# Kernel optimization log

Measured on AMD Instinct MI355X. Metric: run time of the kernel, lower is better.

The kernel has to match this reference:

```python
import jax, jax.numpy as jnp
import numpy as np


def setup_inputs() -> dict:
    key = jax.random.key(0)
    ks = jax.random.split(key, 8)
    B, T, D, S, M = 32, 512, 1024, 256, 10
    scale = 1.0 / np.sqrt(D)
    return {
        "input_h_c": jax.random.normal(ks[0], (B, T, D), dtype=jnp.float32),
        "memory": jax.random.normal(ks[1], (B, S, D), dtype=jnp.float32),
        "input_lengths": jax.random.randint(ks[2], (B,), 1, S),
        "W_ih": jax.random.normal(ks[3], (4 * D, 2 * D), dtype=jnp.float32) * scale,
        "W_hh": jax.random.normal(ks[4], (4 * D, D), dtype=jnp.float32) * scale,
        "b_ih": jnp.zeros((4 * D,), dtype=jnp.float32),
        "b_hh": jnp.zeros((4 * D,), dtype=jnp.float32),
        "W_g": jax.random.normal(ks[5], (3 * M, D), dtype=jnp.float32) * scale,
        "b_g": jnp.zeros((3 * M,), dtype=jnp.float32),
    }


def reference(input_h_c, memory, input_lengths, W_ih, W_hh, b_ih, b_hh, W_g, b_g):
    B, T, D = input_h_c.shape
    S = memory.shape[1]
    M = W_g.shape[0] // 3
    u = jnp.arange(S, dtype=jnp.float32)
    u_R = u + 0.5  # [S]
    u_L = u - 0.5

    def step(carry, inp_t):
        h, c, ksi, ctx = carry
        x = jnp.concatenate([inp_t, ctx], axis=-1)  # [B, 2D]
        gates = x @ W_ih.T + b_ih + h @ W_hh.T + b_hh  # [B, 4D]
        i_g, f_g, g_g, o_g = jnp.split(gates, 4, axis=-1)
        c = jax.nn.sigmoid(f_g) * c + jax.nn.sigmoid(i_g) * jnp.tanh(g_g)
        h = jax.nn.sigmoid(o_g) * jnp.tanh(c)
        phi = h @ W_g.T + b_g  # [B, 3M]
        ksi = jnp.minimum(ksi + jnp.exp(phi[:, :M]), S - 1.0)
        beta = jnp.exp(phi[:, M:2 * M])
        alpha = jax.nn.softmax(phi[:, 2 * M:], axis=-1)
        # F(u) = 1/(1+exp((ksi-u)/beta)) = sigmoid((u-ksi)/beta)
        ks_e = ksi[:, :, None]   # [B,M,1]
        be_e = beta[:, :, None]
        term1 = jnp.einsum('bm,bms->bs', alpha, jax.nn.sigmoid((u_R - ks_e) / be_e))
        term2 = jnp.einsum('bm,bms->bs', alpha, jax.nn.sigmoid((u_L - ks_e) / be_e))
        w = term1 - term2  # [B,S]
        w = w / jnp.sum(w, axis=-1, keepdims=True)
        ctx = jnp.einsum('bs,bsd->bd', w, memory)  # [B,D]
        terminate = 1.0 - term1  # [B,S]
        return (h, c, ksi, ctx), (ctx, w, terminate)

    init = (jnp.zeros((B, D), input_h_c.dtype), jnp.zeros((B, D), input_h_c.dtype),
            jnp.zeros((B, M), input_h_c.dtype), jnp.zeros((B, D), input_h_c.dtype))
    (h, c, ksi, ctx), (ctxs, ws, terms) = jax.lax.scan(step, init, jnp.swapaxes(input_h_c, 0, 1))
    alignment = jnp.swapaxes(ws, 0, 1)  # [B,T,S]
    term_last = terms[-1]  # [B,S] (last timestep, as in torch loop)
    idx = jnp.clip(input_lengths - 1, 0, memory.shape[1] - 1)
    termination = jnp.take_along_axis(term_last, idx[:, None], axis=1)  # [B,1]
    return (ctx[:, None, :], alignment, termination)
```

## Files before the change

### kernel.cpp

```cpp
#include <hip/hip_runtime.h>
#include <cstdint>
#include <cstddef>

#define B_   32
#define T_   512
#define D_   1024
#define S_   256
#define M_   10
#define G4   4096
#define K3   3072
#define NBLK 256
#define NTHR 256

#define AL_OFF   32768
#define TERM_OFF (32768 + (size_t)B_*T_*S_)

__device__ __forceinline__ void gbar(unsigned* bar, unsigned g) {
    __syncthreads();
    if (threadIdx.x == 0) {
        __threadfence();
        const int grp = blockIdx.x & 7;
        unsigned* cnt  = bar + 32*grp;
        unsigned* cntm = bar + 256;
        unsigned* gen  = bar + 512 + 32*grp;
        bool done = false;
        unsigned old = __hip_atomic_fetch_add(cnt, 1u, __ATOMIC_ACQ_REL, __HIP_MEMORY_SCOPE_AGENT);
        if (old == 31u) {
            unsigned old2 = __hip_atomic_fetch_add(cntm, 1u, __ATOMIC_ACQ_REL, __HIP_MEMORY_SCOPE_AGENT);
            if (old2 == 7u) {
                for (int i = 0; i < 8; ++i)
                    __hip_atomic_store(bar + 32*i, 0u, __ATOMIC_RELAXED, __HIP_MEMORY_SCOPE_AGENT);
                __hip_atomic_store(cntm, 0u, __ATOMIC_RELAXED, __HIP_MEMORY_SCOPE_AGENT);
                for (int i = 0; i < 8; ++i)
                    __hip_atomic_store(bar + 512 + 32*i, g + 1u, __ATOMIC_RELEASE, __HIP_MEMORY_SCOPE_AGENT);
                done = true;
            }
        }
        if (!done) {
            while (__hip_atomic_load(gen, __ATOMIC_RELAXED, __HIP_MEMORY_SCOPE_AGENT) == g)
                __builtin_amdgcn_s_sleep(2);
        }
        __threadfence();
    }
    __syncthreads();
}

__global__ __launch_bounds__(256) void k_pack(const float* __restrict__ Wih,
                                              const float* __restrict__ Whh,
                                              float* __restrict__ WrecT) {
    const int kt = blockIdx.x;
    const int jt = blockIdx.y;
    __shared__ float Tt[32][33];
    const int r = threadIdx.x >> 3;
    const int q = threadIdx.x & 7;
    const int j = jt*32 + r;
    const int k = kt*32 + q*4;
    float4 v;
    if (k < 2048) v = *(const float4*)&Wih[(size_t)j*2048 + k];
    else          v = *(const float4*)&Whh[(size_t)j*1024 + (k - 2048)];
    Tt[r][q*4+0] = v.x; Tt[r][q*4+1] = v.y; Tt[r][q*4+2] = v.z; Tt[r][q*4+3] = v.w;
    __syncthreads();
    float4 o;
    o.x = Tt[q*4+0][r]; o.y = Tt[q*4+1][r]; o.z = Tt[q*4+2][r]; o.w = Tt[q*4+3][r];
    *(float4*)&WrecT[(size_t)(kt*32 + r)*G4 + jt*32 + q*4] = o;
}

__global__ __launch_bounds__(256) void k_bsum(const float* __restrict__ bih,
                                              const float* __restrict__ bhh,
                                              float* __restrict__ bsum,
                                              unsigned* __restrict__ bar) {
    int i = blockIdx.x*256 + threadIdx.x;
    if (i < G4) bsum[i] = bih[i] + bhh[i];
    if (blockIdx.x == 0)
        for (int j = threadIdx.x; j < 1024; j += 256) bar[j] = 0u;
}

__global__ __launch_bounds__(NTHR, 1) void k_rec(
    const float* __restrict__ inp,
    const float* __restrict__ mem,
    const int*   __restrict__ lens,
    const float* __restrict__ Wg,
    const float* __restrict__ bg,
    const float* __restrict__ WrecT,
    const float* __restrict__ bsum,
    float* __restrict__ xh,
    float* __restrict__ cst,
    float* __restrict__ ksi,
    float* __restrict__ part,
    float* __restrict__ wcur,
    unsigned* __restrict__ bar,
    float* __restrict__ out)
{
    __shared__ __align__(16) float smem[5632];
    const int blk = blockIdx.x;
    const int tid = threadIdx.x;
    unsigned bgen = 0;

    if (blk < B_) {
        for (int i = tid; i < 2*D_; i += NTHR) xh[blk*2*D_ + i] = 0.f;
        for (int i = tid; i < D_; i += NTHR)   cst[blk*D_ + i]  = 0.f;
        if (tid < M_) ksi[blk*16 + tid] = 0.f;
    }
    gbar(bar, bgen); ++bgen;

    for (int t = 0; t < T_; ++t) {
        {
            const int kc = blk & 7;
            const int jb = blk >> 3;
            const int jbase = jb * 128;
            const int tx = tid & 31;
            const int ty = tid >> 5;
            const int sb = tid >> 3;
            const int sk = tid & 7;
            float* Ws = smem;
            float* Xs = smem + 32*132;
            float acc[4][4] = {{0.f}};
            float4 xv, wv[4];

            auto loadX = [&](int kbase) {
                if (kbase < D_) xv = *(const float4*)&inp[((size_t)sb*T_ + t)*D_ + kbase + sk*4];
                else            xv = *(const float4*)&xh[sb*2*D_ + (kbase - D_) + sk*4];
            };
            auto loadW = [&](int kbase) {
                #pragma unroll
                for (int r = 0; r < 4; ++r) {
                    int id2 = tid + NTHR*r;
                    int wk = id2 >> 5;
                    int wj = (id2 & 31) << 2;
                    wv[r] = *(const float4*)&WrecT[(size_t)(kbase + wk)*G4 + jbase + wj];
                }
            };

            loadX(kc*384); loadW(kc*384);
            for (int kt2 = 0; kt2 < 12; ++kt2) {
                __syncthreads();
                Xs[(sk*4+0)*36 + sb] = xv.x;
                Xs[(sk*4+1)*36 + sb] = xv.y;
                Xs[(sk*4+2)*36 + sb] = xv.z;
                Xs[(sk*4+3)*36 + sb] = xv.w;
                #pragma unroll
                for (int r = 0; r < 4; ++r) {
                    int id2 = tid + NTHR*r;
                    int wk = id2 >> 5;
                    int wj = (id2 & 31) << 2;
                    *(float4*)&Ws[wk*132 + wj] = wv[r];
                }
                __syncthreads();
                if (kt2 < 11) { loadX(kc*384 + (kt2+1)*32); loadW(kc*384 + (kt2+1)*32); }
                #pragma unroll
                for (int kk = 0; kk < 32; ++kk) {
                    float4 wr = *(const float4*)&Ws[kk*132 + (tx<<2)];
                    float4 xr = *(const float4*)&Xs[kk*36  + (ty<<2)];
                    acc[0][0] += xr.x*wr.x; acc[0][1] += xr.x*wr.y; acc[0][2] += xr.x*wr.z; acc[0][3] += xr.x*wr.w;
                    acc[1][0] += xr.y*wr.x; acc[1][1] += xr.y*wr.y; acc[1][2] += xr.y*wr.z; acc[1][3] += xr.y*wr.w;
                    acc[2][0] += xr.z*wr.x; acc[2][1] += xr.z*wr.y; acc[2][2] += xr.z*wr.z; acc[2][3] += xr.z*wr.w;
                    acc[3][0] += xr.w*wr.x; acc[3][1] += xr.w*wr.y; acc[3][2] += xr.w*wr.z; acc[3][3] += xr.w*wr.w;
                }
            }
            #pragma unroll
            for (int i = 0; i < 4; ++i) {
                int b = (ty<<2) + i;
                *(float4*)&part[(size_t)(kc*B_ + b)*G4 + jbase + (tx<<2)] =
                    make_float4(acc[i][0], acc[i][1], acc[i][2], acc[i][3]);
            }
        }
        gbar(bar, bgen); ++bgen;

        if (blk < B_) {
            const int b = blk;
            float* gl = smem;
            float* hl = smem + 4096;
            float* sm = smem + 5120;
            for (int j = tid; j < G4; j += NTHR) {
                float s = bsum[j];
                #pragma unroll
                for (int kc = 0; kc < 8; ++kc) s += part[(size_t)(kc*B_ + b)*G4 + j];
                gl[j] = s;
            }
            __syncthreads();
            for (int d = tid; d < D_; d += NTHR) {
                float ig = 1.f/(1.f + expf(-gl[d]));
                float fg = 1.f/(1.f + expf(-gl[D_ + d]));
                float gg = tanhf(gl[2*D_ + d]);
                float og = 1.f/(1.f + expf(-gl[3*D_ + d]));
                float cn = fg*cst[b*D_ + d] + ig*gg;
                float hn = og*tanhf(cn);
                cst[b*D_ + d] = cn;
                hl[d] = hn;
                xh[b*2*D_ + D_ + d] = hn;
            }
            __syncthreads();
            {
                int m = tid >> 3, l = tid & 7;
                if (m < 30) {
                    float a = 0.f;
                    for (int d0 = l; d0 < D_; d0 += 8) a += hl[d0]*Wg[m*D_ + d0];
                    a += __shfl_down(a, 4, 8);
                    a += __shfl_down(a, 2, 8);
                    a += __shfl_down(a, 1, 8);
                    if (l == 0) sm[m] = a + bg[m];
                }
            }
            __syncthreads();
            if (tid < M_) {
                int mm = tid;
                sm[32+mm] = expf(sm[20+mm]);
                float kn = fminf(ksi[b*16+mm] + expf(sm[mm]), (float)(S_-1));
                ksi[b*16+mm] = kn;
                sm[48+mm] = kn;
                sm[64+mm] = expf(sm[10+mm]);
            }
            if (tid == 0) {
                float se = 0.f;
                #pragma unroll
                for (int mm = 0; mm < M_; ++mm) se += expf(sm[20+mm]);
                sm[88] = se;
            }
            __syncthreads();
            {
                int s = tid;
                float t1 = 0.f, t2 = 0.f;
                #pragma unroll
                for (int mm = 0; mm < M_; ++mm) {
                    float a = sm[32+mm], kk = sm[48+mm], be = sm[64+mm];
                    float xr = ((float)s + 0.5f - kk)/be;
                    float xl = ((float)s - 0.5f - kk)/be;
                    t1 += a/(1.f + expf(-xr));
                    t2 += a/(1.f + expf(-xl));
                }
                float wraw = t1 - t2;
                float v = wraw;
                v += __shfl_down(v, 32); v += __shfl_down(v, 16); v += __shfl_down(v, 8);
                v += __shfl_down(v, 4);  v += __shfl_down(v, 2);  v += __shfl_down(v, 1);
                if ((tid & 63) == 0) sm[96 + (tid >> 6)] = v;
                __syncthreads();
                float wsum = sm[96] + sm[97] + sm[98] + sm[99];
                float w = wraw / wsum;
                wcur[b*S_ + s] = w;
                out[AL_OFF + ((size_t)b*T_ + t)*S_ + s] = w;
                if (t == T_-1) {
                    int idx = lens[b] - 1;
                    idx = idx < 0 ? 0 : (idx > S_-1 ? S_-1 : idx);
                    if (s == idx) out[TERM_OFF + b] = 1.f - t1/sm[88];
                }
            }
        }
        gbar(bar, bgen); ++bgen;

        {
            const int b  = blk & 31;
            const int dc = blk >> 5;
            float* wl  = smem;
            float* red = smem + 256;
            wl[tid] = wcur[b*S_ + tid];
            __syncthreads();
            const int dd = tid & 127;
            const int sh = tid >> 7;
            const int d  = dc*128 + dd;
            const float* mp = mem + ((size_t)b*S_ + sh*128)*D_ + d;
            float acc = 0.f;
            #pragma unroll 8
            for (int s2 = 0; s2 < 128; ++s2) acc += wl[sh*128 + s2] * mp[(size_t)s2*D_];
            if (sh) red[dd] = acc;
            __syncthreads();
            if (!sh) {
                float v = acc + red[dd];
                xh[b*2*D_ + d] = v;
                if (t == T_-1) out[(size_t)b*D_ + d] = v;
            }
        }
        gbar(bar, bgen); ++bgen;
    }
}

extern "C" void kernel_launch(void* const* d_in, const int* in_sizes, int n_in,
                              void* d_out, int out_size, void* d_ws, size_t ws_size,
                              hipStream_t stream) {
    const float* inp  = (const float*)d_in[0];
    const float* mem  = (const float*)d_in[1];
    const int*   lens = (const int*)  d_in[2];
    const float* Wih  = (const float*)d_in[3];
    const float* Whh  = (const float*)d_in[4];
    const float* bih  = (const float*)d_in[5];
    const float* bhh  = (const float*)d_in[6];
    const float* Wg   = (const float*)d_in[7];
    const float* bg   = (const float*)d_in[8];
    float* out = (float*)d_out;

    float* WrecT = (float*)d_ws;
    float* part  = WrecT + (size_t)K3*G4;
    float* xh    = part + (size_t)8*B_*G4;
    float* cst   = xh + B_*2*D_;
    float* ksi   = cst + B_*D_;
    float* wcur  = ksi + B_*16;
    float* bsum  = wcur + B_*S_;
    unsigned* bar = (unsigned*)(bsum + G4);
    size_t need = (size_t)((char*)(bar + 1024) - (char*)d_ws);
    if (ws_size < need) return;

    hipLaunchKernelGGL(k_pack, dim3(96,128), dim3(256), 0, stream, Wih, Whh, WrecT);
    hipLaunchKernelGGL(k_bsum, dim3(16), dim3(256), 0, stream, bih, bhh, bsum, bar);

    void* args[] = { (void*)&inp, (void*)&mem, (void*)&lens, (void*)&Wg, (void*)&bg,
                     (void*)&WrecT, (void*)&bsum, (void*)&xh, (void*)&cst, (void*)&ksi,
                     (void*)&part, (void*)&wcur, (void*)&bar, (void*)&out };
    hipError_t e = hipLaunchCooperativeKernel((void*)k_rec, dim3(NBLK), dim3(NTHR),
                                              args, 0, stream);
    if (e != hipSuccess) {
        hipLaunchKernelGGL(k_rec, dim3(NBLK), dim3(NTHR), 0, stream,
                           inp, mem, lens, Wg, bg, WrecT, bsum, xh, cst, ksi,
                           part, wcur, bar, out);
    }
}
```

Baseline: 58.53 ms.

## Keep LSTM weights register-resident and replicate attention per block to drop a grid barrier

```diff
diff --git a/kernel.cpp b/kernel.cpp
--- a/kernel.cpp
+++ b/kernel.cpp
@@ -14,6 +14,8 @@
 
 #define AL_OFF   32768
 #define TERM_OFF (32768 + (size_t)B_*T_*S_)
+
+#define XS_STRIDE 400
 
 __device__ __forceinline__ void gbar(unsigned* bar, unsigned g) {
     __syncthreads();
@@ -84,189 +86,226 @@
     const float* __restrict__ WrecT,
     const float* __restrict__ bsum,
     float* __restrict__ xh,
-    float* __restrict__ cst,
-    float* __restrict__ ksi,
     float* __restrict__ part,
-    float* __restrict__ wcur,
     unsigned* __restrict__ bar,
     float* __restrict__ out)
 {
-    __shared__ __align__(16) float smem[5632];
+    __shared__ __align__(16) float Xs[B_*XS_STRIDE];
+    __shared__ __align__(16) float hl[D_];
+    __shared__ float wl[S_];
+    __shared__ float sm[128];
+    __shared__ float red[128];
+    __shared__ float ksi_l[16];
+
     const int blk = blockIdx.x;
     const int tid = threadIdx.x;
+    const int kc = blk & 7;
+    const int jb = blk >> 3;
+    const int tk = tid & 7;
+    const int tj = tid >> 3;
+    const int j0 = jb*128 + tj*4;
+    const int b2 = blk & 31;
+    const int dc = blk >> 5;
     unsigned bgen = 0;
 
-    if (blk < B_) {
-        for (int i = tid; i < 2*D_; i += NTHR) xh[blk*2*D_ + i] = 0.f;
-        for (int i = tid; i < D_; i += NTHR)   cst[blk*D_ + i]  = 0.f;
-        if (tid < M_) ksi[blk*16 + tid] = 0.f;
+    float Wreg[192];
+    {
+        const int kb = kc*384 + tk*48;
+        #pragma unroll
+        for (int kk = 0; kk < 48; ++kk) {
+            float4 w4 = *(const float4*)&WrecT[(size_t)(kb + kk)*G4 + j0];
+            Wreg[kk*4+0] = w4.x; Wreg[kk*4+1] = w4.y;
+            Wreg[kk*4+2] = w4.z; Wreg[kk*4+3] = w4.w;
+        }
     }
+    float4 bs4[4];
+    #pragma unroll
+    for (int g = 0; g < 4; ++g) bs4[g] = *(const float4*)&bsum[g*D_ + tid*4];
+
+    float creg[4] = {0.f, 0.f, 0.f, 0.f};
+
+    if (blk < B_) for (int i = tid; i < 2*D_; i += NTHR) xh[blk*2*D_ + i] = 0.f;
+    if (tid < 16) ksi_l[tid] = 0.f;
     gbar(bar, bgen); ++bgen;
 
+    const int colb = tk*48 + 4*((tk>>1)&3);
+
     for (int t = 0; t < T_; ++t) {
-        {
-            const int kc = blk & 7;
-            const int jb = blk >> 3;
-            const int jbase = jb * 128;
-            const int tx = tid & 31;
-            const int ty = tid >> 5;
-            const int sb = tid >> 3;
-            const int sk = tid & 7;
-            float* Ws = smem;
-            float* Xs = smem + 32*132;
-            float acc[4][4] = {{0.f}};
-            float4 xv, wv[4];
-
-            auto loadX = [&](int kbase) {
-                if (kbase < D_) xv = *(const float4*)&inp[((size_t)sb*T_ + t)*D_ + kbase + sk*4];
-                else            xv = *(const float4*)&xh[sb*2*D_ + (kbase - D_) + sk*4];
-            };
-            auto loadW = [&](int kbase) {
-                #pragma unroll
-                for (int r = 0; r < 4; ++r) {
-                    int id2 = tid + NTHR*r;
-                    int wk = id2 >> 5;
-                    int wj = (id2 & 31) << 2;
-                    wv[r] = *(const float4*)&WrecT[(size_t)(kbase + wk)*G4 + jbase + wj];
-                }
-            };
-
-            loadX(kc*384); loadW(kc*384);
-            for (int kt2 = 0; kt2 < 12; ++kt2) {
-                __syncthreads();
-                Xs[(sk*4+0)*36 + sb] = xv.x;
-                Xs[(sk*4+1)*36 + sb] = xv.y;
-                Xs[(sk*4+2)*36 + sb] = xv.z;
-                Xs[(sk*4+3)*36 + sb] = xv.w;
-                #pragma unroll
-                for (int r = 0; r < 4; ++r) {
-                    int id2 = tid + NTHR*r;
-                    int wk = id2 >> 5;
-                    int wj = (id2 & 31) << 2;
-                    *(float4*)&Ws[wk*132 + wj] = wv[r];
-                }
-                __syncthreads();
-                if (kt2 < 11) { loadX(kc*384 + (kt2+1)*32); loadW(kc*384 + (kt2+1)*32); }
-                #pragma unroll
-                for (int kk = 0; kk < 32; ++kk) {
-                    float4 wr = *(const float4*)&Ws[kk*132 + (tx<<2)];
-                    float4 xr = *(const float4*)&Xs[kk*36  + (ty<<2)];
-                    acc[0][0] += xr.x*wr.x; acc[0][1] += xr.x*wr.y; acc[0][2] += xr.x*wr.z; acc[0][3] += xr.x*wr.w;
-                    acc[1][0] += xr.y*wr.x; acc[1][1] += xr.y*wr.y; acc[1][2] += xr.y*wr.z; acc[1][3] += xr.y*wr.w;
-                    acc[2][0] += xr.z*wr.x; acc[2][1] += xr.z*wr.y; acc[2][2] += xr.z*wr.z; acc[2][3] += xr.z*wr.w;
-                    acc[3][0] += xr.w*wr.x; acc[3][1] += xr.w*wr.y; acc[3][2] += xr.w*wr.z; acc[3][3] += xr.w*wr.w;
+        #pragma unroll
+        for (int it = 0; it < 12; ++it) {
+            int fid = it*NTHR + tid;
+            int b   = fid / 96;
+            int k4  = fid - b*96;
+            int k   = kc*384 + k4*4;
+            float4 v;
+            if (k < D_) v = *(const float4*)&inp[((size_t)b*T_ + t)*D_ + k];
+            else        v = *(const float4*)&xh[b*2*D_ + (k - D_)];
+            int col = k4*4 + 4*((k4/24)&3);
+            *(float4*)&Xs[b*XS_STRIDE + col] = v;
+        }
+        __syncthreads();
+        for (int bq = 0; bq < 8; ++bq) {
+            float acc[4][4] = {{0.f,0.f,0.f,0.f},{0.f,0.f,0.f,0.f},
+                               {0.f,0.f,0.f,0.f},{0.f,0.f,0.f,0.f}};
+            const float* x0 = &Xs[(bq*4+0)*XS_STRIDE + colb];
+            const float* x1 = &Xs[(bq*4+1)*XS_STRIDE + colb];
+            const float* x2 = &Xs[(bq*4+2)*XS_STRIDE + colb];
+            const float* x3 = &Xs[(bq*4+3)*XS_STRIDE + colb];
+            #pragma unroll
+            for (int kq = 0; kq < 12; ++kq) {
+                float4 f0 = *(const float4*)(x0 + kq*4);
+                float4 f1 = *(const float4*)(x1 + kq*4);
+                float4 f2 = *(const float4*)(x2 + kq*4);
+                float4 f3 = *(const float4*)(x3 + kq*4);
+                const float* W0 = &Wreg[kq*16];
+                #pragma unroll
+                for (int jj = 0; jj < 4; ++jj) {
+                    float w = W0[jj];
+                    acc[0][jj] += f0.x*w; acc[1][jj] += f1.x*w;
+                    acc[2][jj] += f2.x*w; acc[3][jj] += f3.x*w;
+                }
+                #pragma unroll
+                for (int jj = 0; jj < 4; ++jj) {
+                    float w = W0[4+jj];
+                    acc[0][jj] += f0.y*w; acc[1][jj] += f1.y*w;
+                    acc[2][jj] += f2.y*w; acc[3][jj] += f3.y*w;
+                }
+                #pragma unroll
+                for (int jj = 0; jj < 4; ++jj) {
+                    float w = W0[8+jj];
+                    acc[0][jj] += f0.z*w; acc[1][jj] += f1.z*w;
+                    acc[2][jj] += f2.z*w; acc[3][jj] += f3.z*w;
+                }
+                #pragma unroll
+                for (int jj = 0; jj < 4; ++jj) {
+                    float w = W0[12+jj];
+                    acc[0][jj] += f0.w*w; acc[1][jj] += f1.w*w;
+                    acc[2][jj] += f2.w*w; acc[3][jj] += f3.w*w;
                 }
             }
             #pragma unroll
             for (int i = 0; i < 4; ++i) {
-                int b = (ty<<2) + i;
-                *(float4*)&part[(size_t)(kc*B_ + b)*G4 + jbase + (tx<<2)] =
-                    make_float4(acc[i][0], acc[i][1], acc[i][2], acc[i][3]);
+                #pragma unroll
+                for (int jj = 0; jj < 4; ++jj) {
+                    float v = acc[i][jj];
+                    v += __shfl_xor(v, 1);
+                    v += __shfl_xor(v, 2);
+                    v += __shfl_xor(v, 4);
+                    acc[i][jj] = v;
+                }
+            }
+            if (tk == 0) {
+                #pragma unroll
+                for (int i = 0; i < 4; ++i) {
+                    int b = bq*4 + i;
+                    *(float4*)&part[(size_t)(kc*B_ + b)*G4 + j0] =
+                        make_float4(acc[i][0], acc[i][1], acc[i][2], acc[i][3]);
+                }
             }
         }
         gbar(bar, bgen); ++bgen;
 
-        if (blk < B_) {
-            const int b = blk;
-            float* gl = smem;
-            float* hl = smem + 4096;
-            float* sm = smem + 5120;
-            for (int j = tid; j < G4; j += NTHR) {
-                float s = bsum[j];
-                #pragma unroll
-                for (int kc = 0; kc < 8; ++kc) s += part[(size_t)(kc*B_ + b)*G4 + j];
-                gl[j] = s;
-            }
+        {
+            const int d4 = tid*4;
+            float hv[4];
+            {
+                float ga[4][4];
+                #pragma unroll
+                for (int g = 0; g < 4; ++g) {
+                    float4 s = bs4[g];
+                    #pragma unroll
+                    for (int kc2 = 0; kc2 < 8; ++kc2) {
+                        float4 p = *(const float4*)&part[(size_t)(kc2*B_ + b2)*G4 + g*D_ + d4];
+                        s.x += p.x; s.y += p.y; s.z += p.z; s.w += p.w;
+                    }
+                    ga[g][0] = s.x; ga[g][1] = s.y; ga[g][2] = s.z; ga[g][3] = s.w;
+                }
+                #pragma unroll
+                for (int i = 0; i < 4; ++i) {
+                    float ig = 1.f/(1.f + expf(-ga[0][i]));
+                    float fg = 1.f/(1.f + expf(-ga[1][i]));
+                    float gg = tanhf(ga[2][i]);
+                    float og = 1.f/(1.f + expf(-ga[3][i]));
+                    float cn = fg*creg[i] + ig*gg;
+                    creg[i] = cn;
+                    hv[i] = og*tanhf(cn);
+                }
+            }
+            *(float4*)&hl[d4] = make_float4(hv[0], hv[1], hv[2], hv[3]);
+            if (blk < B_) *(float4*)&xh[b2*2*D_ + D_ + d4] = make_float4(hv[0], hv[1], hv[2], hv[3]);
+        }
+        __syncthreads();
+        {
+            int m = tid >> 3, l = tid & 7;
+            if (m < 30) {
+                float a = 0.f;
+                const float* wgp = &Wg[m*D_];
+                for (int d0 = l; d0 < D_; d0 += 8) a += hl[d0]*wgp[d0];
+                a += __shfl_down(a, 4, 8);
+                a += __shfl_down(a, 2, 8);
+                a += __shfl_down(a, 1, 8);
+                if (l == 0) sm[m] = a + bg[m];
+            }
+        }
+        __syncthreads();
+        if (tid < M_) {
+            sm[32+tid] = expf(sm[20+tid]);
+            float kn = fminf(ksi_l[tid] + expf(sm[tid]), (float)(S_-1));
+            ksi_l[tid] = kn;
+            sm[48+tid] = kn;
+            sm[64+tid] = expf(sm[10+tid]);
+        }
+        if (tid == 0) {
+            float se = 0.f;
+            #pragma unroll
+            for (int mm = 0; mm < M_; ++mm) se += expf(sm[20+mm]);
+            sm[88] = se;
+        }
+        __syncthreads();
+        {
+            int s = tid;
+            float t1 = 0.f, t2 = 0.f;
+            #pragma unroll
+            for (int mm = 0; mm < M_; ++mm) {
+                float a = sm[32+mm], kk2 = sm[48+mm], be = sm[64+mm];
+                float xr = ((float)s + 0.5f - kk2)/be;
+                float xl = ((float)s - 0.5f - kk2)/be;
+                t1 += a/(1.f + expf(-xr));
+                t2 += a/(1.f + expf(-xl));
+            }
+            float wraw = t1 - t2;
+            float v = wraw;
+            v += __shfl_down(v, 32); v += __shfl_down(v, 16); v += __shfl_down(v, 8);
+            v += __shfl_down(v, 4);  v += __shfl_down(v, 2);  v += __shfl_down(v, 1);
+            if ((tid & 63) == 0) sm[96 + (tid >> 6)] = v;
             __syncthreads();
-            for (int d = tid; d < D_; d += NTHR) {
-                float ig = 1.f/(1.f + expf(-gl[d]));
-                float fg = 1.f/(1.f + expf(-gl[D_ + d]));
-                float gg = tanhf(gl[2*D_ + d]);
-                float og = 1.f/(1.f + expf(-gl[3*D_ + d]));
-                float cn = fg*cst[b*D_ + d] + ig*gg;
-                float hn = og*tanhf(cn);
-                cst[b*D_ + d] = cn;
-                hl[d] = hn;
-                xh[b*2*D_ + D_ + d] = hn;
-            }
-            __syncthreads();
-            {
-                int m = tid >> 3, l = tid & 7;
-                if (m < 30) {
-                    float a = 0.f;
-                    for (int d0 = l; d0 < D_; d0 += 8) a += hl[d0]*Wg[m*D_ + d0];
-                    a += __shfl_down(a, 4, 8);
-                    a += __shfl_down(a, 2, 8);
-                    a += __shfl_down(a, 1, 8);
-                    if (l == 0) sm[m] = a + bg[m];
-                }
-            }
-            __syncthreads();
-            if (tid < M_) {
-                int mm = tid;
-                sm[32+mm] = expf(sm[20+mm]);
-                float kn = fminf(ksi[b*16+mm] + expf(sm[mm]), (float)(S_-1));
-                ksi[b*16+mm] = kn;
-                sm[48+mm] = kn;
-                sm[64+mm] = expf(sm[10+mm]);
-            }
-            if (tid == 0) {
-                float se = 0.f;
-                #pragma unroll
-                for (int mm = 0; mm < M_; ++mm) se += expf(sm[20+mm]);
-                sm[88] = se;
-            }
-            __syncthreads();
-            {
-                int s = tid;
-                float t1 = 0.f, t2 = 0.f;
-                #pragma unroll
-                for (int mm = 0; mm < M_; ++mm) {
-                    float a = sm[32+mm], kk = sm[48+mm], be = sm[64+mm];
-                    float xr = ((float)s + 0.5f - kk)/be;
-                    float xl = ((float)s - 0.5f - kk)/be;
-                    t1 += a/(1.f + expf(-xr));
-                    t2 += a/(1.f + expf(-xl));
-                }
-                float wraw = t1 - t2;
-                float v = wraw;
-                v += __shfl_down(v, 32); v += __shfl_down(v, 16); v += __shfl_down(v, 8);
-                v += __shfl_down(v, 4);  v += __shfl_down(v, 2);  v += __shfl_down(v, 1);
-                if ((tid & 63) == 0) sm[96 + (tid >> 6)] = v;
-                __syncthreads();
-                float wsum = sm[96] + sm[97] + sm[98] + sm[99];
-                float w = wraw / wsum;
-                wcur[b*S_ + s] = w;
-                out[AL_OFF + ((size_t)b*T_ + t)*S_ + s] = w;
+            float wsum = sm[96] + sm[97] + sm[98] + sm[99];
+            float w = wraw / wsum;
+            wl[s] = w;
+            if (blk < B_) {
+                out[AL_OFF + ((size_t)b2*T_ + t)*S_ + s] = w;
                 if (t == T_-1) {
-                    int idx = lens[b] - 1;
+                    int idx = lens[b2] - 1;
                     idx = idx < 0 ? 0 : (idx > S_-1 ? S_-1 : idx);
-                    if (s == idx) out[TERM_OFF + b] = 1.f - t1/sm[88];
-                }
-            }
-        }
-        gbar(bar, bgen); ++bgen;
-
+                    if (s == idx) out[TERM_OFF + b2] = 1.f - t1/sm[88];
+                }
+            }
+        }
+        __syncthreads();
         {
-            const int b  = blk & 31;
-            const int dc = blk >> 5;
-            float* wl  = smem;
-            float* red = smem + 256;
-            wl[tid] = wcur[b*S_ + tid];
-            __syncthreads();
             const int dd = tid & 127;
             const int sh = tid >> 7;
             const int d  = dc*128 + dd;
-            const float* mp = mem + ((size_t)b*S_ + sh*128)*D_ + d;
-            float acc = 0.f;
+            const float* mp = mem + ((size_t)b2*S_ + sh*128)*D_ + d;
+            float a3 = 0.f;
             #pragma unroll 8
-            for (int s2 = 0; s2 < 128; ++s2) acc += wl[sh*128 + s2] * mp[(size_t)s2*D_];
-            if (sh) red[dd] = acc;
+            for (int s2 = 0; s2 < 128; ++s2) a3 += wl[sh*128 + s2]*mp[(size_t)s2*D_];
+            if (sh) red[dd] = a3;
             __syncthreads();
             if (!sh) {
-                float v = acc + red[dd];
-                xh[b*2*D_ + d] = v;
-                if (t == T_-1) out[(size_t)b*D_ + d] = v;
+                float v = a3 + red[dd];
+                xh[b2*2*D_ + d] = v;
+                if (t == T_-1) out[(size_t)b2*D_ + d] = v;
             }
         }
         gbar(bar, bgen); ++bgen;
@@ -290,10 +329,7 @@
     float* WrecT = (float*)d_ws;
     float* part  = WrecT + (size_t)K3*G4;
     float* xh    = part + (size_t)8*B_*G4;
-    float* cst   = xh + B_*2*D_;
-    float* ksi   = cst + B_*D_;
-    float* wcur  = ksi + B_*16;
-    float* bsum  = wcur + B_*S_;
+    float* bsum  = xh + (size_t)B_*2*D_;
     unsigned* bar = (unsigned*)(bsum + G4);
     size_t need = (size_t)((char*)(bar + 1024) - (char*)d_ws);
     if (ws_size < need) return;
@@ -302,13 +338,13 @@
     hipLaunchKernelGGL(k_bsum, dim3(16), dim3(256), 0, stream, bih, bhh, bsum, bar);
 
     void* args[] = { (void*)&inp, (void*)&mem, (void*)&lens, (void*)&Wg, (void*)&bg,
-                     (void*)&WrecT, (void*)&bsum, (void*)&xh, (void*)&cst, (void*)&ksi,
-                     (void*)&part, (void*)&wcur, (void*)&bar, (void*)&out };
+                     (void*)&WrecT, (void*)&bsum, (void*)&xh,
+                     (void*)&part, (void*)&bar, (void*)&out };
     hipError_t e = hipLaunchCooperativeKernel((void*)k_rec, dim3(NBLK), dim3(NTHR),
                                               args, 0, stream);
     if (e != hipSuccess) {
         hipLaunchKernelGGL(k_rec, dim3(NBLK), dim3(NTHR), 0, stream,
-                           inp, mem, lens, Wg, bg, WrecT, bsum, xh, cst, ksi,
-                           part, wcur, bar, out);
+                           inp, mem, lens, Wg, bg, WrecT, bsum, xh,
+                           part, bar, out);
     }
 }
```

Measured after the change: 56.55 ms. 1.04x faster.
